# Kernel optimization log

Measured on AMD Instinct MI355X. Metric: run time of the kernel, lower is better.

The kernel has to match this reference:

```python
import jax, jax.numpy as jnp
import numpy as np

# Fixed problem sizes (equal-sized batch segments, matching setup_inputs)
B, N, M = 4, 4096, 16384          # clouds, coarse pts/cloud, fine pts/cloud
C_IN, C_SKIP, K = 256, 256, 3     # feature dims, knn k
CH = [C_IN + C_SKIP, 512, 256]    # MLP channels
EPS = 1e-16


def setup_inputs() -> dict:
    key = jax.random.key(0)
    ks = jax.random.split(key, 6)
    x = jax.random.normal(ks[0], (B * N, C_IN), jnp.float32)
    pos = jax.random.uniform(ks[1], (B * N, 3), jnp.float32)
    batch = jnp.repeat(jnp.arange(B, dtype=jnp.int64), N)
    x_skip = jax.random.normal(ks[2], (B * M, C_SKIP), jnp.float32)
    pos_skip = jax.random.uniform(ks[3], (B * M, 3), jnp.float32)
    batch_skip = jnp.repeat(jnp.arange(B, dtype=jnp.int64), M)
    W1 = jax.random.normal(ks[4], (CH[0], CH[1]), jnp.float32) / np.sqrt(CH[0]).astype(np.float32)
    b1 = jnp.zeros((CH[1],), jnp.float32)
    W2 = jax.random.normal(ks[5], (CH[1], CH[2]), jnp.float32) / np.sqrt(CH[1]).astype(np.float32)
    b2 = jnp.zeros((CH[2],), jnp.float32)
    return dict(x=x, pos=pos, batch=batch, x_skip=x_skip, pos_skip=pos_skip,
                batch_skip=batch_skip, W1=W1, b1=b1, W2=W2, b2=b2)


def _knn_interpolate(x, pos, pos_skip):
    """torch_geometric.nn.knn_interpolate with equal-sized batch segments."""
    xb = x.reshape(B, N, C_IN)
    ps = pos.reshape(B, N, 3)
    qs = pos_skip.reshape(B, M, 3)
    # squared pairwise distances [B, M, N]
    d2 = (jnp.sum(qs * qs, -1)[:, :, None]
          - 2.0 * jnp.einsum('bmd,bnd->bmn', qs, ps)
          + jnp.sum(ps * ps, -1)[:, None, :])
    neg_d2, idx = jax.lax.top_k(-d2, K)                # k smallest distances, [B,M,K]
    w = 1.0 / jnp.clip(-neg_d2, EPS)                   # inverse squared distance weights
    feats = jax.vmap(lambda f, i: f[i])(xb, idx)       # gather: [B, M, K, C_IN]
    y = jnp.sum(w[..., None] * feats, axis=2) / jnp.sum(w, axis=2)[..., None]
    return y.reshape(B * M, C_IN)


def reference(x, pos, batch, x_skip, pos_skip, batch_skip, W1, b1, W2, b2):
    y = _knn_interpolate(x, pos, pos_skip)
    h = jnp.concatenate([y, x_skip], axis=1)           # [B*M, 512]
    h = jax.nn.relu(h @ W1 + b1)
    h = jax.nn.relu(h @ W2 + b2)
    return h, pos_skip, batch_skip
```

## Files before the change

### kernel.cpp

```cpp
#include <hip/hip_runtime.h>
#include <stdint.h>

#define NB 4
#define NPTS 4096
#define MPTS 16384
#define CIN 256
#define CH0 512
#define CH1 512
#define CH2 256
#define ROWS (NB * MPTS)
#define POS_OUT_OFF (ROWS * CH2)
#define BATCH_OUT_OFF (POS_OUT_OFF + ROWS * 3)
#define CELL_CAP 40
#define QCAP 96

using u16 = unsigned short;
using u32 = unsigned int;
using u64 = unsigned long long;

typedef __bf16 bf16x8 __attribute__((ext_vector_type(8)));
typedef float f32x4 __attribute__((ext_vector_type(4)));

__device__ __forceinline__ u16 f2bf(float f) {
  u32 u = __builtin_bit_cast(u32, f);
  u32 r = u + 0x7fffu + ((u >> 16) & 1u);
  return (u16)(r >> 16);
}

__device__ __forceinline__ u32 flipf(float f) {
  u32 u = __builtin_bit_cast(u32, f);
  return u ^ ((u32)((int)u >> 31) | 0x80000000u);
}
__device__ __forceinline__ float unflipf(u32 f) {
  u32 m = (~(u32)((int)f >> 31)) | 0x80000000u;
  return __builtin_bit_cast(float, f ^ m);
}

__device__ __forceinline__ void ins3(u64 v, u64& k0, u64& k1, u64& k2) {
  u64 a = k0 < v ? v : k0;
  k0 = k0 < v ? k0 : v;
  u64 bb = k1 < a ? a : k1;
  k1 = k1 < a ? k1 : a;
  k2 = k2 < bb ? k2 : bb;
}

__device__ __forceinline__ void merge3(u64 r0, u64 r1, u64 r2,
                                       u64& k0, u64& k1, u64& k2) {
  u64 t = k0 < r0 ? r0 : k0;
  k0 = k0 < r0 ? k0 : r0;
  u64 u = k1 < r1 ? k1 : r1;
  u64 mtu = t < u ? u : t;
  k1 = t < u ? t : u;
  u64 v = k2 < r2 ? k2 : r2;
  k2 = mtu < v ? mtu : v;
}

__device__ __forceinline__ u64 shfl_xor_u64_w8(u64 v, int mask) {
  u32 lo = (u32)v, hi = (u32)(v >> 32);
  lo = (u32)__shfl_xor((int)lo, mask, 8);
  hi = (u32)__shfl_xor((int)hi, mask, 8);
  return ((u64)hi << 32) | lo;
}

__global__ __launch_bounds__(256) void prep_kernel(
    const float* __restrict__ W1, const float* __restrict__ W2,
    u16* __restrict__ W1T, u16* __restrict__ W2T) {
  int t = blockIdx.x * 256 + threadIdx.x;
  if (t < CH0 * CH1) {
    int n = t >> 9, k = t & 511;
    W1T[t] = f2bf(W1[k * CH1 + n]);
  } else {
    int u = t - CH0 * CH1;
    int n = u >> 9, k = u & 511;
    W2T[u] = f2bf(W2[k * CH2 + n]);
  }
}

__global__ __launch_bounds__(256) void tail_kernel(
    const float* __restrict__ pos_skip, const int* __restrict__ batch_skip,
    float* __restrict__ out) {
  int t = blockIdx.x * 256 + threadIdx.x;
  if (t < ROWS * 3) {
    out[POS_OUT_OFF + t] = pos_skip[t];
  } else {
    int u = t - ROWS * 3;
    out[BATCH_OUT_OFF + u] = (float)batch_skip[u];
  }
}

__global__ __launch_bounds__(256) void build_kernel(
    const float* __restrict__ pos, float4* __restrict__ pts4,
    u32* __restrict__ cellCnt, int* __restrict__ cellIdx) {
#pragma clang fp contract(off)
  const int i = blockIdx.x * 256 + threadIdx.x;
  const float x = pos[i * 3 + 0], y = pos[i * 3 + 1], z = pos[i * 3 + 2];
  pts4[i] = make_float4(x, y, z, (x * x + y * y) + z * z);
  const int b = i >> 12;
  int cx = (int)(x * 8.0f); cx = cx < 0 ? 0 : (cx > 7 ? 7 : cx);
  int cy = (int)(y * 8.0f); cy = cy < 0 ? 0 : (cy > 7 ? 7 : cy);
  int cz = (int)(z * 8.0f); cz = cz < 0 ? 0 : (cz > 7 ? 7 : cz);
  const int c = b * 512 + cz * 64 + cy * 8 + cx;
  const u32 slot = atomicAdd(&cellCnt[c], 1u);
  if (slot < CELL_CAP) cellIdx[c * CELL_CAP + slot] = i;
}

__global__ __launch_bounds__(256) void qbin_kernel(
    const float* __restrict__ pos_skip, u32* __restrict__ qCnt,
    int* __restrict__ qIdx) {
  const int q = blockIdx.x * 256 + threadIdx.x;
  const int b = q >> 14;
  const float qx = pos_skip[q * 3 + 0];
  const float qy = pos_skip[q * 3 + 1];
  const float qz = pos_skip[q * 3 + 2];
  int cx = (int)(qx * 8.0f); cx = cx < 0 ? 0 : (cx > 7 ? 7 : cx);
  int cy = (int)(qy * 8.0f); cy = cy < 0 ? 0 : (cy > 7 ? 7 : cy);
  int cz = (int)(qz * 8.0f); cz = cz < 0 ? 0 : (cz > 7 ? 7 : cz);
  const int c = b * 512 + cz * 64 + cy * 8 + cx;
  const u32 slot = atomicAdd(&qCnt[c], 1u);
  if (slot < QCAP) qIdx[c * QCAP + slot] = q;
}

__global__ __launch_bounds__(256) void knn_kernel(
    const float4* __restrict__ pts4, const u32* __restrict__ cellCnt,
    const int* __restrict__ cellIdx, const u32* __restrict__ qCnt,
    const int* __restrict__ qIdx, const float* __restrict__ pos_skip,
    int* __restrict__ idx_out, float* __restrict__ w_out) {
#pragma clang fp contract(off)
  __shared__ float4 scand[27 * CELL_CAP];
  __shared__ int    scgi[27 * CELL_CAP];
  __shared__ u32    scnt[27];
  __shared__ int    sbase[27];
  __shared__ u32    nCand;
  const int tid = threadIdx.x;
  const int b = blockIdx.x >> 9;
  const int cell = blockIdx.x & 511;
  const int cz = cell >> 6, cy = (cell >> 3) & 7, cx = cell & 7;
  const int x0 = cx > 0 ? cx - 1 : 0, x1 = cx < 7 ? cx + 1 : 7;
  const int y0 = cy > 0 ? cy - 1 : 0, y1 = cy < 7 ? cy + 1 : 7;
  const int z0 = cz > 0 ? cz - 1 : 0, z1 = cz < 7 ? cz + 1 : 7;
  const int nx = x1 - x0 + 1, ny = y1 - y0 + 1, nz = z1 - z0 + 1;
  const int ncells = nx * ny * nz;
  if (tid == 0) nCand = 0;
  if (tid < ncells) {
    const int lz = tid / (nx * ny);
    const int rem = tid - lz * nx * ny;
    const int ly = rem / nx;
    const int lx = rem - ly * nx;
    const int cg = b * 512 + (z0 + lz) * 64 + (y0 + ly) * 8 + (x0 + lx);
    u32 cnt = cellCnt[cg];
    scnt[tid] = cnt > CELL_CAP ? CELL_CAP : cnt;
    sbase[tid] = cg * CELL_CAP;
  }
  __syncthreads();
  const int slots = ncells * CELL_CAP;
  for (int s = tid; s < slots; s += 256) {
    const int ci = s / CELL_CAP;
    const int sl = s - ci * CELL_CAP;
    if ((u32)sl < scnt[ci]) {
      const int gi = cellIdx[sbase[ci] + sl];
      const float4 p = pts4[gi];
      const u32 d = atomicAdd(&nCand, 1u);
      scand[d] = p;
      scgi[d] = gi;
    }
  }
  __syncthreads();
  const int nC = (int)nCand;
  u32 nq = qCnt[b * 512 + cell];
  if (nq > QCAP) nq = QCAP;
  const int qbase = (b * 512 + cell) * QCAP;
  const int g = tid >> 3;
  const int sub = tid & 7;

  for (int r0q = 0; r0q < (int)nq; r0q += 32) {
    const int qslot = r0q + g;
    if (qslot < (int)nq) {
      const int q = qIdx[qbase + qslot];
      const float qx = pos_skip[q * 3 + 0];
      const float qy = pos_skip[q * 3 + 1];
      const float qz = pos_skip[q * 3 + 2];
      const float q2 = (qx * qx + qy * qy) + qz * qz;
      u64 k0 = ~0ull, k1 = ~0ull, k2 = ~0ull;
      for (int s = sub; s < nC; s += 8) {
        const float4 p = scand[s];
        const float dot = fmaf(qz, p.z, fmaf(qy, p.y, qx * p.x));
        const float tv = (q2 - 2.0f * dot) + p.w;
        const u64 key = ((u64)flipf(tv) << 32) | (u32)scgi[s];
        ins3(key, k0, k1, k2);
      }
#pragma unroll
      for (int mask = 1; mask < 8; mask <<= 1) {
        const u64 r0 = shfl_xor_u64_w8(k0, mask);
        const u64 r1 = shfl_xor_u64_w8(k1, mask);
        const u64 r2 = shfl_xor_u64_w8(k2, mask);
        merge3(r0, r1, r2, k0, k1, k2);
      }
      float m2tv = unflipf((u32)(k2 >> 32));
      if (!(m2tv <= 0.015625f - 1e-5f)) {
        k0 = k1 = k2 = ~0ull;
        const int ex0 = cx > 1 ? cx - 2 : 0, ex1 = cx < 6 ? cx + 2 : 7;
        const int ey0 = cy > 1 ? cy - 2 : 0, ey1 = cy < 6 ? cy + 2 : 7;
        const int ez0 = cz > 1 ? cz - 2 : 0, ez1 = cz < 6 ? cz + 2 : 7;
        for (int zz = ez0; zz <= ez1; ++zz)
          for (int yy = ey0; yy <= ey1; ++yy)
            for (int xx = ex0; xx <= ex1; ++xx) {
              const int cg = b * 512 + zz * 64 + yy * 8 + xx;
              u32 cnt = cellCnt[cg];
              if (cnt > CELL_CAP) cnt = CELL_CAP;
              const int cb = cg * CELL_CAP;
              for (int s = sub; s < (int)cnt; s += 8) {
                const int gi = cellIdx[cb + s];
                const float4 p = pts4[gi];
                const float dot = fmaf(qz, p.z, fmaf(qy, p.y, qx * p.x));
                const float tv = (q2 - 2.0f * dot) + p.w;
                ins3(((u64)flipf(tv) << 32) | (u32)gi, k0, k1, k2);
              }
            }
#pragma unroll
        for (int mask = 1; mask < 8; mask <<= 1) {
          const u64 r0 = shfl_xor_u64_w8(k0, mask);
          const u64 r1 = shfl_xor_u64_w8(k1, mask);
          const u64 r2 = shfl_xor_u64_w8(k2, mask);
          merge3(r0, r1, r2, k0, k1, k2);
        }
        m2tv = unflipf((u32)(k2 >> 32));
        if (!(m2tv <= 0.0625f - 1e-5f)) {
          k0 = k1 = k2 = ~0ull;
          const int base = b * NPTS;
          for (int i = sub; i < NPTS; i += 8) {
            const int gi = base + i;
            const float4 p = pts4[gi];
            const float dot = fmaf(qz, p.z, fmaf(qy, p.y, qx * p.x));
            const float tv = (q2 - 2.0f * dot) + p.w;
            ins3(((u64)flipf(tv) << 32) | (u32)gi, k0, k1, k2);
          }
#pragma unroll
          for (int mask = 1; mask < 8; mask <<= 1) {
            const u64 r0 = shfl_xor_u64_w8(k0, mask);
            const u64 r1 = shfl_xor_u64_w8(k1, mask);
            const u64 r2 = shfl_xor_u64_w8(k2, mask);
            merge3(r0, r1, r2, k0, k1, k2);
          }
        }
      }
      if (sub == 0) {
        const float t0 = unflipf((u32)(k0 >> 32));
        const float t1 = unflipf((u32)(k1 >> 32));
        const float t2 = unflipf((u32)(k2 >> 32));
        const int j0 = (int)(u32)k0;
        const int j1 = (int)(u32)k1;
        const int j2 = (int)(u32)k2;
        const float w0 = 1.0f / fmaxf(t0, 1e-16f);
        const float w1 = 1.0f / fmaxf(t1, 1e-16f);
        const float w2 = 1.0f / fmaxf(t2, 1e-16f);
        const float wsum = (w0 + w1) + w2;
        const float inv = 1.0f / wsum;
        idx_out[q * 3 + 0] = j0;
        idx_out[q * 3 + 1] = j1;
        idx_out[q * 3 + 2] = j2;
        w_out[q * 3 + 0] = w0 * inv;
        w_out[q * 3 + 1] = w1 * inv;
        w_out[q * 3 + 2] = w2 * inv;
      }
    }
  }
}

__global__ __launch_bounds__(256) void interp_kernel(
    const float* __restrict__ x, const int* __restrict__ idx,
    const float* __restrict__ w, const float* __restrict__ x_skip,
    u16* __restrict__ H) {
  const int row = blockIdx.x * 4 + (threadIdx.x >> 6);
  const int lane = threadIdx.x & 63;
  const int i0 = idx[row * 3 + 0], i1 = idx[row * 3 + 1], i2 = idx[row * 3 + 2];
  const float w0 = w[row * 3 + 0], w1 = w[row * 3 + 1], w2 = w[row * 3 + 2];
  const float4 a0 = ((const float4*)(x + (size_t)i0 * CIN))[lane];
  const float4 a1 = ((const float4*)(x + (size_t)i1 * CIN))[lane];
  const float4 a2 = ((const float4*)(x + (size_t)i2 * CIN))[lane];
  const float4 s  = ((const float4*)(x_skip + (size_t)row * CIN))[lane];
  float y0 = fmaf(w0, a0.x, fmaf(w1, a1.x, w2 * a2.x));
  float y1 = fmaf(w0, a0.y, fmaf(w1, a1.y, w2 * a2.y));
  float y2 = fmaf(w0, a0.z, fmaf(w1, a1.z, w2 * a2.z));
  float y3 = fmaf(w0, a0.w, fmaf(w1, a1.w, w2 * a2.w));
  u16* rp = H + (size_t)row * CH0;
  u32 lo = (u32)f2bf(y0) | ((u32)f2bf(y1) << 16);
  u32 hi = (u32)f2bf(y2) | ((u32)f2bf(y3) << 16);
  *(uint2*)(rp + lane * 4) = make_uint2(lo, hi);
  lo = (u32)f2bf(s.x) | ((u32)f2bf(s.y) << 16);
  hi = (u32)f2bf(s.z) | ((u32)f2bf(s.w) << 16);
  *(uint2*)(rp + CIN + lane * 4) = make_uint2(lo, hi);
}

__device__ __forceinline__ void gload_lds16(const u16* g, u16* l) {
  __builtin_amdgcn_global_load_lds(
      (__attribute__((address_space(1))) void*)g,
      (__attribute__((address_space(3))) void*)l, 16, 0, 0);
}

template <int KD, int ND, bool OUT_BF16>
__global__ __launch_bounds__(256) void gemm_kernel(
    const u16* __restrict__ A, const u16* __restrict__ Bt,
    const float* __restrict__ bias, void* __restrict__ Cout) {
  __shared__ __align__(16) u16 As[128 * 32];
  __shared__ __align__(16) u16 Bs[128 * 32];
  const int wid = threadIdx.x >> 6;
  const int lane = threadIdx.x & 63;
  const size_t arow0 = (size_t)blockIdx.x * 128;
  const size_t brow0 = (size_t)blockIdx.y * 128;
  const int c0 = wid * 2, c1 = wid * 2 + 1;
  const int lr = lane >> 2;
  const int lk = (lane & 3) * 8;
  const u16* gA0 = A + (arow0 + c0 * 16 + lr) * KD + lk;
  const u16* gA1 = A + (arow0 + c1 * 16 + lr) * KD + lk;
  const u16* gB0 = Bt + (brow0 + c0 * 16 + lr) * KD + lk;
  const u16* gB1 = Bt + (brow0 + c1 * 16 + lr) * KD + lk;
  u16* lA0 = As + c0 * 512 + lane * 8;
  u16* lA1 = As + c1 * 512 + lane * 8;
  u16* lB0 = Bs + c0 * 512 + lane * 8;
  u16* lB1 = Bs + c1 * 512 + lane * 8;

  f32x4 acc[4][4];
#pragma unroll
  for (int mi = 0; mi < 4; mi++)
#pragma unroll
    for (int ni = 0; ni < 4; ni++) acc[mi][ni] = (f32x4){0.f, 0.f, 0.f, 0.f};

  const int wr = (wid >> 1) * 64;
  const int wc = (wid & 1) * 64;
  const int fr = lane & 15;
  const int fk = (lane >> 4) * 8;

  for (int k0 = 0; k0 < KD; k0 += 32) {
    gload_lds16(gA0 + k0, lA0);
    gload_lds16(gA1 + k0, lA1);
    gload_lds16(gB0 + k0, lB0);
    gload_lds16(gB1 + k0, lB1);
    __syncthreads();
    bf16x8 af[4], bfr[4];
#pragma unroll
    for (int mi = 0; mi < 4; mi++)
      af[mi] = *(const bf16x8*)&As[(wr + mi * 16 + fr) * 32 + fk];
#pragma unroll
    for (int ni = 0; ni < 4; ni++)
      bfr[ni] = *(const bf16x8*)&Bs[(wc + ni * 16 + fr) * 32 + fk];
#pragma unroll
    for (int mi = 0; mi < 4; mi++)
#pragma unroll
      for (int ni = 0; ni < 4; ni++)
        acc[mi][ni] = __builtin_amdgcn_mfma_f32_16x16x32_bf16(
            af[mi], bfr[ni], acc[mi][ni], 0, 0, 0);
    __syncthreads();
  }

  const int rbase = (int)arow0 + wr + (lane >> 4) * 4;
  const int cbase = (int)brow0 + wc + fr;
#pragma unroll
  for (int ni = 0; ni < 4; ni++) {
    const int colg = cbase + ni * 16;
    const float bc = bias[colg];
#pragma unroll
    for (int mi = 0; mi < 4; mi++) {
#pragma unroll
      for (int r = 0; r < 4; r++) {
        float v = fmaxf(acc[mi][ni][r] + bc, 0.f);
        const size_t o = (size_t)(rbase + mi * 16 + r) * ND + colg;
        if constexpr (OUT_BF16) ((u16*)Cout)[o] = f2bf(v);
        else                    ((float*)Cout)[o] = v;
      }
    }
  }
}

extern "C" void kernel_launch(void* const* d_in, const int* in_sizes, int n_in,
                              void* d_out, int out_size, void* d_ws, size_t ws_size,
                              hipStream_t stream) {
  const float* x        = (const float*)d_in[0];
  const float* pos      = (const float*)d_in[1];
  const float* x_skip   = (const float*)d_in[3];
  const float* pos_skip = (const float*)d_in[4];
  const int*   batch_sk = (const int*)d_in[5];
  const float* W1       = (const float*)d_in[6];
  const float* b1       = (const float*)d_in[7];
  const float* W2       = (const float*)d_in[8];
  const float* b2       = (const float*)d_in[9];
  float* out = (float*)d_out;

  char* ws = (char*)d_ws;
  u16*   W1T  = (u16*)(ws);
  u16*   W2T  = (u16*)(ws + 524288);
  int*   idxb = (int*)(ws + 786432);
  float* wb   = (float*)(ws + 1572864);
  u16*   Hcat = (u16*)(ws + 2359296);
  u16*   H1   = (u16*)(ws + 69468160);
  float4* pts4    = (float4*)(ws + 132382720);
  u32*    cellCnt = (u32*)(ws + 132644864);
  u32*    qCnt    = (u32*)(ws + 132653056);
  int*    cellIdx = (int*)(ws + 132661248);
  int*    qIdx    = (int*)(ws + 132988928);

  hipMemsetAsync(cellCnt, 0, 16384, stream);
  prep_kernel<<<dim3(1536), dim3(256), 0, stream>>>(W1, W2, W1T, W2T);
  tail_kernel<<<dim3(1024), dim3(256), 0, stream>>>(pos_skip, batch_sk, out);
  build_kernel<<<dim3(64), dim3(256), 0, stream>>>(pos, pts4, cellCnt, cellIdx);
  qbin_kernel<<<dim3(256), dim3(256), 0, stream>>>(pos_skip, qCnt, qIdx);
  knn_kernel<<<dim3(2048), dim3(256), 0, stream>>>(pts4, cellCnt, cellIdx,
                                                   qCnt, qIdx, pos_skip,
                                                   idxb, wb);
  interp_kernel<<<dim3(16384), dim3(256), 0, stream>>>(x, idxb, wb, x_skip, Hcat);
  gemm_kernel<CH0, CH1, true><<<dim3(ROWS / 128, CH1 / 128), dim3(256), 0, stream>>>(
      Hcat, W1T, b1, (void*)H1);
  gemm_kernel<CH1, CH2, false><<<dim3(ROWS / 128, CH2 / 128), dim3(256), 0, stream>>>(
      H1, W2T, b2, (void*)out);
}
```

Measured before the change: 299.5 us.

## Fuse interpolation and both MLP GEMMs into one LDS-resident kernel

Replaces the separate interpolation kernel and two GEMM kernels with one fused kernel. Each block builds a 64-row bf16 concatenated activation tile in swizzled LDS, runs both layers, and keeps the hidden activations in LDS. Weights are pre-packed into MFMA fragment order so they stream straight from global memory into registers with double buffering. This removes the Hcat and H1 round trips through HBM and two launches. In exchange, each block uses 64KB of LDS, occupancy is lower, weights are reloaded per block from L2, and there is no LDS pipelining of A.

```diff
diff --git a/kernel.cpp b/kernel.cpp
--- a/kernel.cpp
+++ b/kernel.cpp
@@ -64,15 +64,27 @@
 
 __global__ __launch_bounds__(256) void prep_kernel(
     const float* __restrict__ W1, const float* __restrict__ W2,
-    u16* __restrict__ W1T, u16* __restrict__ W2T) {
-  int t = blockIdx.x * 256 + threadIdx.x;
-  if (t < CH0 * CH1) {
-    int n = t >> 9, k = t & 511;
-    W1T[t] = f2bf(W1[k * CH1 + n]);
+    u16* __restrict__ W1s, u16* __restrict__ W2s) {
+  const int t = blockIdx.x * 256 + threadIdx.x;
+  if (t < 32768) {
+    const int l = t & 63, ni = (t >> 6) & 3, wd = (t >> 8) & 7, kt = t >> 11;
+    const int fr = l & 15, g = l >> 4;
+    const int n = wd * 64 + ni * 16 + fr;
+    u16 o[8];
+#pragma unroll
+    for (int j = 0; j < 8; ++j)
+      o[j] = f2bf(W1[(kt * 32 + g * 8 + j) * CH1 + n]);
+    *(uint4*)(W1s + (size_t)t * 8) = *(const uint4*)o;
   } else {
-    int u = t - CH0 * CH1;
-    int n = u >> 9, k = u & 511;
-    W2T[u] = f2bf(W2[k * CH2 + n]);
+    const int c = t - 32768;
+    const int l = c & 63, ni = (c >> 6) & 1, wd = (c >> 7) & 7, kt = c >> 10;
+    const int fr = l & 15, g = l >> 4;
+    const int n = wd * 32 + ni * 16 + fr;
+    u16 o[8];
+#pragma unroll
+    for (int j = 0; j < 8; ++j)
+      o[j] = f2bf(W2[(kt * 32 + g * 8 + j) * CH2 + n]);
+    *(uint4*)(W2s + (size_t)c * 8) = *(const uint4*)o;
   }
 }
 
@@ -247,17 +259,14 @@
         const float t0 = unflipf((u32)(k0 >> 32));
         const float t1 = unflipf((u32)(k1 >> 32));
         const float t2 = unflipf((u32)(k2 >> 32));
-        const int j0 = (int)(u32)k0;
-        const int j1 = (int)(u32)k1;
-        const int j2 = (int)(u32)k2;
         const float w0 = 1.0f / fmaxf(t0, 1e-16f);
         const float w1 = 1.0f / fmaxf(t1, 1e-16f);
         const float w2 = 1.0f / fmaxf(t2, 1e-16f);
         const float wsum = (w0 + w1) + w2;
         const float inv = 1.0f / wsum;
-        idx_out[q * 3 + 0] = j0;
-        idx_out[q * 3 + 1] = j1;
-        idx_out[q * 3 + 2] = j2;
+        idx_out[q * 3 + 0] = (int)(u32)k0;
+        idx_out[q * 3 + 1] = (int)(u32)k1;
+        idx_out[q * 3 + 2] = (int)(u32)k2;
         w_out[q * 3 + 0] = w0 * inv;
         w_out[q * 3 + 1] = w1 * inv;
         w_out[q * 3 + 2] = w2 * inv;
@@ -266,58 +275,64 @@
   }
 }
 
-__global__ __launch_bounds__(256) void interp_kernel(
+__global__ __launch_bounds__(512, 2) void fused_mlp_kernel(
     const float* __restrict__ x, const int* __restrict__ idx,
     const float* __restrict__ w, const float* __restrict__ x_skip,
-    u16* __restrict__ H) {
-  const int row = blockIdx.x * 4 + (threadIdx.x >> 6);
-  const int lane = threadIdx.x & 63;
-  const int i0 = idx[row * 3 + 0], i1 = idx[row * 3 + 1], i2 = idx[row * 3 + 2];
-  const float w0 = w[row * 3 + 0], w1 = w[row * 3 + 1], w2 = w[row * 3 + 2];
-  const float4 a0 = ((const float4*)(x + (size_t)i0 * CIN))[lane];
-  const float4 a1 = ((const float4*)(x + (size_t)i1 * CIN))[lane];
-  const float4 a2 = ((const float4*)(x + (size_t)i2 * CIN))[lane];
-  const float4 s  = ((const float4*)(x_skip + (size_t)row * CIN))[lane];
-  float y0 = fmaf(w0, a0.x, fmaf(w1, a1.x, w2 * a2.x));
-  float y1 = fmaf(w0, a0.y, fmaf(w1, a1.y, w2 * a2.y));
-  float y2 = fmaf(w0, a0.z, fmaf(w1, a1.z, w2 * a2.z));
-  float y3 = fmaf(w0, a0.w, fmaf(w1, a1.w, w2 * a2.w));
-  u16* rp = H + (size_t)row * CH0;
-  u32 lo = (u32)f2bf(y0) | ((u32)f2bf(y1) << 16);
-  u32 hi = (u32)f2bf(y2) | ((u32)f2bf(y3) << 16);
-  *(uint2*)(rp + lane * 4) = make_uint2(lo, hi);
-  lo = (u32)f2bf(s.x) | ((u32)f2bf(s.y) << 16);
-  hi = (u32)f2bf(s.z) | ((u32)f2bf(s.w) << 16);
-  *(uint2*)(rp + CIN + lane * 4) = make_uint2(lo, hi);
-}
-
-__device__ __forceinline__ void gload_lds16(const u16* g, u16* l) {
-  __builtin_amdgcn_global_load_lds(
-      (__attribute__((address_space(1))) void*)g,
-      (__attribute__((address_space(3))) void*)l, 16, 0, 0);
-}
-
-template <int KD, int ND, bool OUT_BF16>
-__global__ __launch_bounds__(256) void gemm_kernel(
-    const u16* __restrict__ A, const u16* __restrict__ Bt,
-    const float* __restrict__ bias, void* __restrict__ Cout) {
-  __shared__ __align__(16) u16 As[128 * 32];
-  __shared__ __align__(16) u16 Bs[128 * 32];
-  const int wid = threadIdx.x >> 6;
-  const int lane = threadIdx.x & 63;
-  const size_t arow0 = (size_t)blockIdx.x * 128;
-  const size_t brow0 = (size_t)blockIdx.y * 128;
-  const int c0 = wid * 2, c1 = wid * 2 + 1;
-  const int lr = lane >> 2;
-  const int lk = (lane & 3) * 8;
-  const u16* gA0 = A + (arow0 + c0 * 16 + lr) * KD + lk;
-  const u16* gA1 = A + (arow0 + c1 * 16 + lr) * KD + lk;
-  const u16* gB0 = Bt + (brow0 + c0 * 16 + lr) * KD + lk;
-  const u16* gB1 = Bt + (brow0 + c1 * 16 + lr) * KD + lk;
-  u16* lA0 = As + c0 * 512 + lane * 8;
-  u16* lA1 = As + c1 * 512 + lane * 8;
-  u16* lB0 = Bs + c0 * 512 + lane * 8;
-  u16* lB1 = Bs + c1 * 512 + lane * 8;
+    const u16* __restrict__ W1s, const float* __restrict__ b1,
+    const u16* __restrict__ W2s, const float* __restrict__ b2,
+    float* __restrict__ out) {
+  __shared__ __align__(16) u16 Abuf[64 * 512];
+  const int tid = threadIdx.x;
+  const int m0 = blockIdx.x * 64;
+
+  {
+    const int row = tid >> 3;
+    const int sub = tid & 7;
+    const int gr = m0 + row;
+    u16* rowp = Abuf + row * 512;
+    const int rx = row & 7;
+    if (sub < 4) {
+      const int i0 = idx[gr * 3 + 0], i1 = idx[gr * 3 + 1], i2 = idx[gr * 3 + 2];
+      const float w0 = w[gr * 3 + 0], w1 = w[gr * 3 + 1], w2 = w[gr * 3 + 2];
+      const float4* p0 = (const float4*)(x + (size_t)i0 * CIN + sub * 64);
+      const float4* p1 = (const float4*)(x + (size_t)i1 * CIN + sub * 64);
+      const float4* p2 = (const float4*)(x + (size_t)i2 * CIN + sub * 64);
+#pragma unroll
+      for (int c = 0; c < 8; ++c) {
+        const float4 a0 = p0[c * 2], a1 = p1[c * 2], a2 = p2[c * 2];
+        const float4 d0 = p0[c * 2 + 1], d1 = p1[c * 2 + 1], d2 = p2[c * 2 + 1];
+        u16 o[8];
+        o[0] = f2bf(fmaf(w0, a0.x, fmaf(w1, a1.x, w2 * a2.x)));
+        o[1] = f2bf(fmaf(w0, a0.y, fmaf(w1, a1.y, w2 * a2.y)));
+        o[2] = f2bf(fmaf(w0, a0.z, fmaf(w1, a1.z, w2 * a2.z)));
+        o[3] = f2bf(fmaf(w0, a0.w, fmaf(w1, a1.w, w2 * a2.w)));
+        o[4] = f2bf(fmaf(w0, d0.x, fmaf(w1, d1.x, w2 * d2.x)));
+        o[5] = f2bf(fmaf(w0, d0.y, fmaf(w1, d1.y, w2 * d2.y)));
+        o[6] = f2bf(fmaf(w0, d0.z, fmaf(w1, d1.z, w2 * d2.z)));
+        o[7] = f2bf(fmaf(w0, d0.w, fmaf(w1, d1.w, w2 * d2.w)));
+        const int vg = sub * 8 + c;
+        *(uint4*)(rowp + (vg ^ rx) * 8) = *(const uint4*)o;
+      }
+    } else {
+      const float4* ps = (const float4*)(x_skip + (size_t)gr * CIN + (sub - 4) * 64);
+#pragma unroll
+      for (int c = 0; c < 8; ++c) {
+        const float4 a = ps[c * 2], d = ps[c * 2 + 1];
+        u16 o[8];
+        o[0] = f2bf(a.x); o[1] = f2bf(a.y); o[2] = f2bf(a.z); o[3] = f2bf(a.w);
+        o[4] = f2bf(d.x); o[5] = f2bf(d.y); o[6] = f2bf(d.z); o[7] = f2bf(d.w);
+        const int vg = 32 + (sub - 4) * 8 + c;
+        *(uint4*)(rowp + (vg ^ rx) * 8) = *(const uint4*)o;
+      }
+    }
+  }
+  __syncthreads();
+
+  const int wid = tid >> 6;
+  const int lane = tid & 63;
+  const int fr = lane & 15;
+  const int g = lane >> 4;
+  const int frx = fr & 7;
 
   f32x4 acc[4][4];
 #pragma unroll
@@ -325,47 +340,100 @@
 #pragma unroll
     for (int ni = 0; ni < 4; ni++) acc[mi][ni] = (f32x4){0.f, 0.f, 0.f, 0.f};
 
-  const int wr = (wid >> 1) * 64;
-  const int wc = (wid & 1) * 64;
-  const int fr = lane & 15;
-  const int fk = (lane >> 4) * 8;
-
-  for (int k0 = 0; k0 < KD; k0 += 32) {
-    gload_lds16(gA0 + k0, lA0);
-    gload_lds16(gA1 + k0, lA1);
-    gload_lds16(gB0 + k0, lB0);
-    gload_lds16(gB1 + k0, lB1);
-    __syncthreads();
-    bf16x8 af[4], bfr[4];
-#pragma unroll
-    for (int mi = 0; mi < 4; mi++)
-      af[mi] = *(const bf16x8*)&As[(wr + mi * 16 + fr) * 32 + fk];
+  {
+    const u16* B1 = W1s + wid * 2048 + lane * 8;
+    bf16x8 bf[2][4];
 #pragma unroll
     for (int ni = 0; ni < 4; ni++)
-      bfr[ni] = *(const bf16x8*)&Bs[(wc + ni * 16 + fr) * 32 + fk];
-#pragma unroll
-    for (int mi = 0; mi < 4; mi++)
-#pragma unroll
-      for (int ni = 0; ni < 4; ni++)
-        acc[mi][ni] = __builtin_amdgcn_mfma_f32_16x16x32_bf16(
-            af[mi], bfr[ni], acc[mi][ni], 0, 0, 0);
-    __syncthreads();
-  }
-
-  const int rbase = (int)arow0 + wr + (lane >> 4) * 4;
-  const int cbase = (int)brow0 + wc + fr;
-#pragma unroll
-  for (int ni = 0; ni < 4; ni++) {
-    const int colg = cbase + ni * 16;
-    const float bc = bias[colg];
+      bf[0][ni] = *(const bf16x8*)(B1 + ni * 512);
+    for (int kt = 0; kt < 16; ++kt) {
+      const int cur = kt & 1;
+      if (kt < 15) {
+        const u16* nb = B1 + (kt + 1) * 16384;
+#pragma unroll
+        for (int ni = 0; ni < 4; ni++)
+          bf[cur ^ 1][ni] = *(const bf16x8*)(nb + ni * 512);
+      }
+      bf16x8 af[4];
+#pragma unroll
+      for (int mi = 0; mi < 4; mi++)
+        af[mi] = *(const bf16x8*)&Abuf[(mi * 16 + fr) * 512 +
+                                       (((kt * 4 + g) ^ frx) * 8)];
+#pragma unroll
+      for (int mi = 0; mi < 4; mi++)
+#pragma unroll
+        for (int ni = 0; ni < 4; ni++)
+          acc[mi][ni] = __builtin_amdgcn_mfma_f32_16x16x32_bf16(
+              af[mi], bf[cur][ni], acc[mi][ni], 0, 0, 0);
+    }
+  }
+  __syncthreads();
+
+  {
+    const int wn = wid * 64;
+#pragma unroll
+    for (int ni = 0; ni < 4; ni++) {
+      const int n = wn + ni * 16 + fr;
+      const float bb = b1[n];
+      const int vg = n >> 3;
+      const int nlow = n & 7;
+#pragma unroll
+      for (int mi = 0; mi < 4; mi++) {
+#pragma unroll
+        for (int r = 0; r < 4; r++) {
+          const int m = mi * 16 + g * 4 + r;
+          const float v = fmaxf(acc[mi][ni][r] + bb, 0.f);
+          Abuf[m * 512 + (vg ^ (m & 7)) * 8 + nlow] = f2bf(v);
+        }
+      }
+    }
+  }
+  __syncthreads();
+
+  f32x4 acc2[4][2];
+#pragma unroll
+  for (int mi = 0; mi < 4; mi++)
+#pragma unroll
+    for (int ni = 0; ni < 2; ni++) acc2[mi][ni] = (f32x4){0.f, 0.f, 0.f, 0.f};
+
+  {
+    const u16* B2 = W2s + wid * 1024 + lane * 8;
+    bf16x8 bf[2][2];
+#pragma unroll
+    for (int ni = 0; ni < 2; ni++)
+      bf[0][ni] = *(const bf16x8*)(B2 + ni * 512);
+    for (int kt = 0; kt < 16; ++kt) {
+      const int cur = kt & 1;
+      if (kt < 15) {
+        const u16* nb = B2 + (kt + 1) * 8192;
+#pragma unroll
+        for (int ni = 0; ni < 2; ni++)
+          bf[cur ^ 1][ni] = *(const bf16x8*)(nb + ni * 512);
+      }
+      bf16x8 af[4];
+#pragma unroll
+      for (int mi = 0; mi < 4; mi++)
+        af[mi] = *(const bf16x8*)&Abuf[(mi * 16 + fr) * 512 +
+                                       (((kt * 4 + g) ^ frx) * 8)];
+#pragma unroll
+      for (int mi = 0; mi < 4; mi++)
+#pragma unroll
+        for (int ni = 0; ni < 2; ni++)
+          acc2[mi][ni] = __builtin_amdgcn_mfma_f32_16x16x32_bf16(
+              af[mi], bf[cur][ni], acc2[mi][ni], 0, 0, 0);
+    }
+  }
+
+#pragma unroll
+  for (int ni = 0; ni < 2; ni++) {
+    const int col = wid * 32 + ni * 16 + fr;
+    const float bb = b2[col];
 #pragma unroll
     for (int mi = 0; mi < 4; mi++) {
 #pragma unroll
       for (int r = 0; r < 4; r++) {
-        float v = fmaxf(acc[mi][ni][r] + bc, 0.f);
-        const size_t o = (size_t)(rbase + mi * 16 + r) * ND + colg;
-        if constexpr (OUT_BF16) ((u16*)Cout)[o] = f2bf(v);
-        else                    ((float*)Cout)[o] = v;
+        const int rowg = m0 + mi * 16 + g * 4 + r;
+        out[(size_t)rowg * CH2 + col] = fmaxf(acc2[mi][ni][r] + bb, 0.f);
       }
     }
   }
@@ -386,29 +454,24 @@
   float* out = (float*)d_out;
 
   char* ws = (char*)d_ws;
-  u16*   W1T  = (u16*)(ws);
-  u16*   W2T  = (u16*)(ws + 524288);
-  int*   idxb = (int*)(ws + 786432);
-  float* wb   = (float*)(ws + 1572864);
-  u16*   Hcat = (u16*)(ws + 2359296);
-  u16*   H1   = (u16*)(ws + 69468160);
-  float4* pts4    = (float4*)(ws + 132382720);
-  u32*    cellCnt = (u32*)(ws + 132644864);
-  u32*    qCnt    = (u32*)(ws + 132653056);
-  int*    cellIdx = (int*)(ws + 132661248);
-  int*    qIdx    = (int*)(ws + 132988928);
+  u16*    W1s     = (u16*)(ws);
+  u16*    W2s     = (u16*)(ws + 524288);
+  int*    idxb    = (int*)(ws + 786432);
+  float*  wb      = (float*)(ws + 1572864);
+  float4* pts4    = (float4*)(ws + 2359296);
+  u32*    cellCnt = (u32*)(ws + 2621440);
+  u32*    qCnt    = (u32*)(ws + 2629632);
+  int*    cellIdx = (int*)(ws + 2637824);
+  int*    qIdx    = (int*)(ws + 2965504);
 
   hipMemsetAsync(cellCnt, 0, 16384, stream);
-  prep_kernel<<<dim3(1536), dim3(256), 0, stream>>>(W1, W2, W1T, W2T);
+  prep_kernel<<<dim3(192), dim3(256), 0, stream>>>(W1, W2, W1s, W2s);
   tail_kernel<<<dim3(1024), dim3(256), 0, stream>>>(pos_skip, batch_sk, out);
   build_kernel<<<dim3(64), dim3(256), 0, stream>>>(pos, pts4, cellCnt, cellIdx);
   qbin_kernel<<<dim3(256), dim3(256), 0, stream>>>(pos_skip, qCnt, qIdx);
   knn_kernel<<<dim3(2048), dim3(256), 0, stream>>>(pts4, cellCnt, cellIdx,
                                                    qCnt, qIdx, pos_skip,
                                                    idxb, wb);
-  interp_kernel<<<dim3(16384), dim3(256), 0, stream>>>(x, idxb, wb, x_skip, Hcat);
-  gemm_kernel<CH0, CH1, true><<<dim3(ROWS / 128, CH1 / 128), dim3(256), 0, stream>>>(
-      Hcat, W1T, b1, (void*)H1);
-  gemm_kernel<CH1, CH2, false><<<dim3(ROWS / 128, CH2 / 128), dim3(256), 0, stream>>>(
-      H1, W2T, b2, (void*)out);
-}
+  fused_mlp_kernel<<<dim3(1024), dim3(512), 0, stream>>>(
+      x, idxb, wb, x_skip, W1s, b1, W2s, b2, out);
+}
```

New measurement: 272.0 us. 9.2% less time.
